# Kernel tuning notes

Hardware: AMD Instinct MI355X
Metric: run time of the kernel (lower is better)

## Reference

```python
import jax, jax.numpy as jnp
import numpy as np

D_MODEL = 1024
N_HEADS = 16
D_K = D_MODEL // N_HEADS


def setup_inputs() -> dict:
    key = jax.random.key(0)
    ks = jax.random.split(key, 9)
    s = 1.0 / np.sqrt(D_MODEL)
    x = jax.random.normal(ks[0], (2, 2048, D_MODEL), dtype=jnp.float32)
    Wq = jax.random.uniform(ks[1], (D_MODEL, D_MODEL), jnp.float32, -s, s)
    bq = jax.random.uniform(ks[2], (D_MODEL,), jnp.float32, -s, s)
    Wk = jax.random.uniform(ks[3], (D_MODEL, D_MODEL), jnp.float32, -s, s)
    bk = jax.random.uniform(ks[4], (D_MODEL,), jnp.float32, -s, s)
    Wv = jax.random.uniform(ks[5], (D_MODEL, D_MODEL), jnp.float32, -s, s)
    bv = jax.random.uniform(ks[6], (D_MODEL,), jnp.float32, -s, s)
    Wo = jax.random.uniform(ks[7], (D_MODEL, D_MODEL), jnp.float32, -s, s)
    bo = jax.random.uniform(ks[8], (D_MODEL,), jnp.float32, -s, s)
    return {"x": x, "Wq": Wq, "bq": bq, "Wk": Wk, "bk": bk,
            "Wv": Wv, "bv": bv, "Wo": Wo, "bo": bo}


def reference(x, Wq, bq, Wk, bk, Wv, bv, Wo, bo):
    B, S, _ = x.shape
    # torch Linear: y = x @ W.T + b
    def proj(W, b):
        h = x @ W.T + b                       # [B,S,D]
        return h.reshape(B, S, N_HEADS, D_K).transpose(0, 2, 1, 3)  # [B,H,S,dk]
    Q, K, V = proj(Wq, bq), proj(Wk, bk), proj(Wv, bv)
    scale = 1.0 / np.sqrt(D_K).astype(np.float32)
    scores = jnp.einsum('bhqd,bhkd->bhqk', Q, K) * scale  # [B,H,S,S]
    causal = jnp.tril(jnp.ones((S, S), dtype=bool))
    scores = jnp.where(causal, scores, -jnp.inf)
    attn = jax.nn.softmax(scores, axis=-1)
    ctx = jnp.einsum('bhqk,bhkd->bhqd', attn, V)          # [B,H,S,dk]
    ctx = ctx.transpose(0, 2, 1, 3).reshape(B, S, D_MODEL)
    return ctx @ Wo.T + bo
```

## Files before the change

### kernel.cpp

```cpp
#include <hip/hip_runtime.h>
#include <stdint.h>

#define D_MODEL 1024
#define NHEADS  16
#define DKH     64
#define BATCH   2
#define SEQ     2048
#define NTOK    (BATCH*SEQ)

typedef unsigned short u16;
typedef __attribute__((ext_vector_type(8))) short short8;
typedef __attribute__((ext_vector_type(4))) float f32x4;
typedef __attribute__((address_space(1))) unsigned int as1_u32;
typedef __attribute__((address_space(3))) unsigned int as3_u32;

__device__ __forceinline__ u16 f2bf(float f) {
  unsigned int i = __float_as_uint(f);
  i += 0x7FFF + ((i >> 16) & 1);
  return (u16)(i >> 16);
}
__device__ __forceinline__ f32x4 mfma_bf16(short8 a, short8 b, f32x4 c) {
  return __builtin_amdgcn_mfma_f32_16x16x32_bf16(a, b, c, 0, 0, 0);
}
__device__ __forceinline__ void gload_lds16(const u16* g, u16* l) {
  __builtin_amdgcn_global_load_lds((as1_u32*)g, (as3_u32*)l, 16, 0, 0);
}
__device__ __forceinline__ short8 ld_frag(const u16* p) {
  short8 v; __builtin_memcpy(&v, __builtin_assume_aligned(p, 16), 16); return v;
}
__device__ __forceinline__ void ld16(uint32_t* dst4, const void* src) {
  __builtin_memcpy(dst4, __builtin_assume_aligned(src, 16), 16);
}
__device__ __forceinline__ void st16(u16* dst, const uint32_t* src4) {
  __builtin_memcpy(__builtin_assume_aligned(dst, 16), src4, 16);
}
__device__ __forceinline__ uint32_t pk_bf16_trunc(float hi, float lo) {
  return __builtin_amdgcn_perm(__float_as_uint(hi), __float_as_uint(lo), 0x07060302u);
}

#define QSCALE 0.18033688011112042f
#define M0LOG2 4.32808512266689f

__global__ __launch_bounds__(256)
void convert_kernel(const float* __restrict__ x,  const float* __restrict__ wq,
                    const float* __restrict__ wk, const float* __restrict__ wv,
                    const float* __restrict__ wo,
                    u16* __restrict__ xb,  u16* __restrict__ wqb,
                    u16* __restrict__ wkb, u16* __restrict__ wvb,
                    u16* __restrict__ wob)
{
  const int q = blockIdx.x * 256 + threadIdx.x;
  const float* src; u16* dst; int local;
  if (q < 1048576) { src = x; dst = xb; local = q; }
  else {
    const int t = q - 1048576, r = t >> 18;
    local = t & 262143;
    src = (r == 0) ? wq : (r == 1) ? wk : (r == 2) ? wv : wo;
    dst = (r == 0) ? wqb : (r == 1) ? wkb : (r == 2) ? wvb : wob;
  }
  float f[4];
  __builtin_memcpy(f, src + (size_t)local * 4, 16);
  uint32_t o[2];
  o[0] = ((uint32_t)f2bf(f[1]) << 16) | f2bf(f[0]);
  o[1] = ((uint32_t)f2bf(f[3]) << 16) | f2bf(f[2]);
  __builtin_memcpy(dst + (size_t)local * 4, o, 8);
}

__device__ __forceinline__ void gemm_core_bf16(
    const u16* __restrict__ A, const u16* __restrict__ Bt,
    int m0, int n0, u16* As, u16* Bs, f32x4 (&acc)[4][4])
{
  const int tid  = threadIdx.x;
  const int wave = tid >> 6, lane = tid & 63;
  const int quad = lane >> 4, l15 = lane & 15;
  const int wm = wave & 1, wn = wave >> 1;
  const int srow = lane >> 2;
  const int scol = (lane & 3) << 3;

#pragma unroll
  for (int i = 0; i < 4; i++)
#pragma unroll
    for (int j = 0; j < 4; j++) acc[i][j] = (f32x4){0.f, 0.f, 0.f, 0.f};

  for (int k0 = 0; k0 < D_MODEL; k0 += 32) {
    __syncthreads();
#pragma unroll
    for (int is = 0; is < 2; is++) {
      const int rbase = (is * 4 + wave) * 16;
      gload_lds16(A  + (size_t)(m0 + rbase + srow) * D_MODEL + k0 + scol, As + rbase * 32);
      gload_lds16(Bt + (size_t)(n0 + rbase + srow) * D_MODEL + k0 + scol, Bs + rbase * 32);
    }
    __syncthreads();

    short8 aF[4], bF[4];
#pragma unroll
    for (int i = 0; i < 4; i++)
      aF[i] = ld_frag(As + (wm * 64 + i * 16 + l15) * 32 + quad * 8);
#pragma unroll
    for (int j = 0; j < 4; j++)
      bF[j] = ld_frag(Bs + (wn * 64 + j * 16 + l15) * 32 + quad * 8);
#pragma unroll
    for (int i = 0; i < 4; i++)
#pragma unroll
      for (int j = 0; j < 4; j++)
        acc[i][j] = mfma_bf16(aF[i], bF[j], acc[i][j]);
  }
}

__global__ __launch_bounds__(256)
void qkv_proj_kernel(const u16* __restrict__ xb,
                     const u16* __restrict__ Wqb, const u16* __restrict__ Wkb,
                     const u16* __restrict__ Wvb,
                     const float* __restrict__ bq, const float* __restrict__ bk,
                     const float* __restrict__ bv,
                     u16* __restrict__ qplane, u16* __restrict__ ws)
{
  __shared__ __align__(16) u16 As[128 * 32];
  __shared__ __align__(16) u16 Bs[128 * 32];

  const int m0  = blockIdx.x * 128;
  const int by  = blockIdx.y;
  const int mat = by >> 3;
  const int n0  = (by & 7) * 128;
  const u16* W      = (mat == 0) ? Wqb : (mat == 1) ? Wkb : Wvb;
  const float* bias = (mat == 0) ? bq : (mat == 1) ? bk : bv;
  u16* out = (mat == 0) ? qplane : ws + (size_t)(mat - 1) * ((size_t)NTOK * D_MODEL);
  const float scale = (mat == 0) ? QSCALE : 1.0f;

  f32x4 acc[4][4];
  gemm_core_bf16(xb, W, m0, n0, As, Bs, acc);

  const int tid = threadIdx.x, wave = tid >> 6, lane = tid & 63;
  const int quad = lane >> 4, l15 = lane & 15;
  const int wm = wave & 1, wn = wave >> 1;
#pragma unroll
  for (int j = 0; j < 4; j++) {
    const int gcol = n0 + wn * 64 + j * 16 + l15;
    const float bias_v = bias[gcol];
    const int h = gcol >> 6, dj = gcol & 63;
#pragma unroll
    for (int i = 0; i < 4; i++) {
#pragma unroll
      for (int r = 0; r < 4; r++) {
        const int grow = m0 + wm * 64 + i * 16 + quad * 4 + r;
        const int b = grow >> 11, s = grow & (SEQ - 1);
        const float v = (acc[i][j][r] + bias_v) * scale;
        out[(((size_t)(b * NHEADS + h)) * SEQ + s) * DKH + dj] = f2bf(v);
      }
    }
  }
}

#define LP 72

__device__ __forceinline__ void storeVt(u16* Vt, const uint32_t* va,
                                        const uint32_t* vb, int r2, int cV) {
#pragma unroll
  for (int j = 0; j < 8; j++) {
    const uint32_t lo = (va[j >> 1] >> (16 * (j & 1))) & 0xFFFFu;
    const uint32_t hi = (vb[j >> 1] >> (16 * (j & 1))) & 0xFFFFu;
    const uint32_t w = (hi << 16) | lo;
    __builtin_memcpy(Vt + (size_t)(cV + j) * LP + r2, &w, 4);
  }
}

__global__ __launch_bounds__(512, 4)
void attn_kernel(const u16* __restrict__ Qp, const u16* __restrict__ Kp,
                 const u16* __restrict__ Vp, u16* __restrict__ ctx)
{
  __shared__ __align__(16) u16 Ks[2][64 * LP];
  __shared__ __align__(16) u16 Vts[2][64 * LP];
  __shared__ __align__(16) u16 PsB[2][64 * LP];
  __shared__ float Ls[2][64];

  const int xp = blockIdx.x;
  const int bh = blockIdx.y;
  const u16* Q = Qp + (size_t)bh * SEQ * DKH;
  const u16* K = Kp + (size_t)bh * SEQ * DKH;
  const u16* V = Vp + (size_t)bh * SEQ * DKH;

  const int tid = threadIdx.x;
  const int wave = tid >> 6, lane = tid & 63;
  const int quad = lane >> 4, l15 = lane & 15;
  const int g    = tid >> 8;
  const int qw   = wave & 3;
  const int ktid = tid & 255;
  const int rK = ktid & 63, cK = (ktid >> 6) * 16;
  const int r2 = (ktid & 31) * 2, cV = (ktid >> 5) * 8;
  const int qloc = qw * 16 + l15;
  const int b = bh >> 4, h = bh & 15;
  u16* Psg = PsB[g];
  float* Osum = (float*)(&PsB[0][0]);

#pragma unroll
  for (int p = 0; p < 2; p++) {
    const int qt = p ? xp : 31 - xp;
    const int q0 = qt * 64;
    const int maxR = (qt >> 1) + 1;

    const short8 qf0 = ld_frag(Q + (size_t)(q0 + qw * 16 + l15) * DKH + quad * 8);
    const short8 qf1 = ld_frag(Q + (size_t)(q0 + qw * 16 + l15) * DKH + 32 + quad * 8);

    uint32_t ka[4], kb[4], va[4], vb[4];
    const bool act0 = (g <= qt);
    if (act0) {
      const int k0 = g * 64;
      ld16(ka, K + (size_t)(k0 + rK) * DKH + cK);
      ld16(kb, K + (size_t)(k0 + rK) * DKH + cK + 8);
      ld16(va, V + (size_t)(k0 + r2) * DKH + cV);
      ld16(vb, V + (size_t)(k0 + r2 + 1) * DKH + cV);
    }
    __syncthreads();
    if (act0) {
      st16(Ks[g] + rK * LP + cK,     ka);
      st16(Ks[g] + rK * LP + cK + 8, kb);
      storeVt(Vts[g], va, vb, r2, cV);
    }
    float l_acc = 0.f;
    f32x4 oacc[4];
#pragma unroll
    for (int td = 0; td < 4; td++) oacc[td] = (f32x4){0.f, 0.f, 0.f, 0.f};
    __syncthreads();

    for (int r = 0; r < maxR; r++) {
      const int kt = 2 * r + g;
      const bool act = (kt <= qt);
      const bool pre = (kt + 2 <= qt);
      if (pre) {
        const int kn = (kt + 2) * 64;
        ld16(ka, K + (size_t)(kn + rK) * DKH + cK);
        ld16(kb, K + (size_t)(kn + rK) * DKH + cK + 8);
        ld16(va, V + (size_t)(kn + r2) * DKH + cV);
        ld16(vb, V + (size_t)(kn + r2 + 1) * DKH + cV);
      }
      if (act) {
        f32x4 sacc[4];
#pragma unroll
        for (int tk = 0; tk < 4; tk++)
          sacc[tk] = (f32x4){-M0LOG2, -M0LOG2, -M0LOG2, -M0LOG2};
#pragma unroll
        for (int tk = 0; tk < 4; tk++) {
          const short8 kf0 = ld_frag(Ks[g] + (tk * 16 + l15) * LP + 0  + quad * 8);
          sacc[tk] = mfma_bf16(kf0, qf0, sacc[tk]);
          const short8 kf1 = ld_frag(Ks[g] + (tk * 16 + l15) * LP + 32 + quad * 8);
          sacc[tk] = mfma_bf16(kf1, qf1, sacc[tk]);
        }
        const bool diag = (kt == qt);
#pragma unroll
        for (int tk = 0; tk < 4; tk++) {
          float pr[4];
#pragma unroll
          for (int rg = 0; rg < 4; rg++) {
            float pv = exp2f(sacc[tk][rg]);
            if (diag) {
              const int kloc = tk * 16 + quad * 4 + rg;
              if (kloc > qloc) pv = 0.f;
            }
            pr[rg] = pv; l_acc += pv;
          }
          uint32_t w[2];
          w[0] = pk_bf16_trunc(pr[1], pr[0]);
          w[1] = pk_bf16_trunc(pr[3], pr[2]);
          __builtin_memcpy(__builtin_assume_aligned(
              Psg + (size_t)(qw * 16 + l15) * LP + tk * 16 + quad * 4, 8), w, 8);
        }
#pragma unroll
        for (int kk = 0; kk < 2; kk++) {
          const short8 pf = ld_frag(Psg + (size_t)(qw * 16 + l15) * LP + kk * 32 + quad * 8);
#pragma unroll
          for (int td = 0; td < 4; td++) {
            const short8 vf = ld_frag(Vts[g] + (size_t)(td * 16 + l15) * LP + kk * 32 + quad * 8);
            oacc[td] = mfma_bf16(pf, vf, oacc[td]);
          }
        }
      }
      if (r + 1 < maxR) {
        __syncthreads();
        if (pre) {
          st16(Ks[g] + rK * LP + cK,     ka);
          st16(Ks[g] + rK * LP + cK + 8, kb);
          storeVt(Vts[g], va, vb, r2, cV);
        }
        __syncthreads();
      }
    }

    l_acc += __shfl_xor(l_acc, 16);
    l_acc += __shfl_xor(l_acc, 32);
    if (quad == 0) Ls[g][qw * 16 + l15] = l_acc;
    __syncthreads();
    if (g == 0) {
#pragma unroll
      for (int td = 0; td < 4; td++)
#pragma unroll
        for (int rg = 0; rg < 4; rg++)
          Osum[(qw * 16 + quad * 4 + rg) * 65 + td * 16 + l15] = oacc[td][rg];
    }
    __syncthreads();
    if (g == 1) {
#pragma unroll
      for (int rg = 0; rg < 4; rg++) {
        const int qrow = qw * 16 + quad * 4 + rg;
        const float inv = 1.0f / (Ls[0][qrow] + Ls[1][qrow]);
        const int sq = q0 + qrow;
#pragma unroll
        for (int td = 0; td < 4; td++) {
          const int dcol = td * 16 + l15;
          const float v = (oacc[td][rg] + Osum[qrow * 65 + dcol]) * inv;
          ctx[((size_t)(b * SEQ + sq)) * D_MODEL + h * DKH + dcol] = f2bf(v);
        }
      }
    }
  }
}

__global__ __launch_bounds__(256)
void oproj_kernel(const u16* __restrict__ ctx, const u16* __restrict__ Wob,
                  const float* __restrict__ bo, float* __restrict__ out)
{
  __shared__ __align__(16) u16 As[128 * 32];
  __shared__ __align__(16) u16 Bs[128 * 32];
  const int m0 = blockIdx.x * 128, n0 = blockIdx.y * 128;

  f32x4 acc[4][4];
  gemm_core_bf16(ctx, Wob, m0, n0, As, Bs, acc);

  const int tid = threadIdx.x, wave = tid >> 6, lane = tid & 63;
  const int quad = lane >> 4, l15 = lane & 15;
  const int wm = wave & 1, wn = wave >> 1;
#pragma unroll
  for (int j = 0; j < 4; j++) {
    const int gcol = n0 + wn * 64 + j * 16 + l15;
    const float bias_v = bo[gcol];
#pragma unroll
    for (int i = 0; i < 4; i++) {
#pragma unroll
      for (int r = 0; r < 4; r++) {
        const int grow = m0 + wm * 64 + i * 16 + quad * 4 + r;
        out[(size_t)grow * D_MODEL + gcol] = acc[i][j][r] + bias_v;
      }
    }
  }
}

extern "C" void kernel_launch(void* const* d_in, const int* in_sizes, int n_in,
                              void* d_out, int out_size, void* d_ws, size_t ws_size,
                              hipStream_t stream) {
  const float* x  = (const float*)d_in[0];
  const float* Wq = (const float*)d_in[1];
  const float* bq = (const float*)d_in[2];
  const float* Wk = (const float*)d_in[3];
  const float* bk = (const float*)d_in[4];
  const float* Wv = (const float*)d_in[5];
  const float* bv = (const float*)d_in[6];
  const float* Wo = (const float*)d_in[7];
  const float* bo = (const float*)d_in[8];
  u16*   ws   = (u16*)d_ws;
  u16*   o16  = (u16*)d_out;
  float* out  = (float*)d_out;

  const size_t plane = (size_t)NTOK * D_MODEL;
  u16* Kp  = ws;
  u16* Vp  = ws + plane;
  u16* xb  = ws + 2 * plane;
  u16* ctx = ws + 2 * plane;
  u16* Wob = ws + 3 * plane;
  u16* Qp  = o16;
  u16* Wqb = o16 + 4 * 1048576;
  u16* Wkb = o16 + 5 * 1048576;
  u16* Wvb = o16 + 6 * 1048576;

  convert_kernel<<<dim3(8192), dim3(256), 0, stream>>>(x, Wq, Wk, Wv, Wo,
                                                       xb, Wqb, Wkb, Wvb, Wob);
  qkv_proj_kernel<<<dim3(32, 24), dim3(256), 0, stream>>>(xb, Wqb, Wkb, Wvb,
                                                          bq, bk, bv, Qp, ws);
  attn_kernel<<<dim3(16, 32), dim3(512), 0, stream>>>(Qp, Kp, Vp, ctx);
  oproj_kernel<<<dim3(32, 8), dim3(256), 0, stream>>>(ctx, Wob, bo, out);
}
```

Before: 209.6 us.

## Restructure attention to 32x32 MFMA with 4-way key split and swizzled LDS

```diff
diff --git a/kernel.cpp b/kernel.cpp
--- a/kernel.cpp
+++ b/kernel.cpp
@@ -11,6 +11,8 @@
 typedef unsigned short u16;
 typedef __attribute__((ext_vector_type(8))) short short8;
 typedef __attribute__((ext_vector_type(4))) float f32x4;
+typedef __attribute__((ext_vector_type(16))) float f32x16;
+typedef __attribute__((ext_vector_type(2))) unsigned int u32x2;
 typedef __attribute__((address_space(1))) unsigned int as1_u32;
 typedef __attribute__((address_space(3))) unsigned int as3_u32;
 
@@ -21,6 +23,9 @@
 }
 __device__ __forceinline__ f32x4 mfma_bf16(short8 a, short8 b, f32x4 c) {
   return __builtin_amdgcn_mfma_f32_16x16x32_bf16(a, b, c, 0, 0, 0);
+}
+__device__ __forceinline__ f32x16 mfma32(short8 a, short8 b, f32x16 c) {
+  return __builtin_amdgcn_mfma_f32_32x32x16_bf16(a, b, c, 0, 0, 0);
 }
 __device__ __forceinline__ void gload_lds16(const u16* g, u16* l) {
   __builtin_amdgcn_global_load_lds((as1_u32*)g, (as3_u32*)l, 16, 0, 0);
@@ -151,16 +156,64 @@
   }
 }
 
-#define LP 72
 
 __device__ __forceinline__ void storeVt(u16* Vt, const uint32_t* va,
                                         const uint32_t* vb, int r2, int cV) {
 #pragma unroll
   for (int j = 0; j < 8; j++) {
+    const int d = cV + j;
     const uint32_t lo = (va[j >> 1] >> (16 * (j & 1))) & 0xFFFFu;
     const uint32_t hi = (vb[j >> 1] >> (16 * (j & 1))) & 0xFFFFu;
     const uint32_t w = (hi << 16) | lo;
-    __builtin_memcpy(Vt + (size_t)(cV + j) * LP + r2, &w, 4);
+    __builtin_memcpy(Vt + d * 64 + (r2 ^ ((d & 7) << 3)), &w, 4);
+  }
+}
+
+__device__ __forceinline__ void soft_pack(const f32x16& s, const int khBase,
+                                          const bool diag, const int qloc,
+                                          const int h4, float& l_acc,
+                                          short8& fA, short8& fB) {
+  float pv[16];
+#pragma unroll
+  for (int rr = 0; rr < 16; rr++) {
+    float v = exp2f(s[rr]);
+    if (diag) {
+      const int kloc = khBase + (rr & 3) + 8 * (rr >> 2) + h4;
+      if (kloc > qloc) v = 0.f;
+    }
+    pv[rr] = v; l_acc += v;
+  }
+  uint32_t w[2][4];
+#pragma unroll
+  for (int ks = 0; ks < 2; ks++) {
+    const uint32_t x0 = pk_bf16_trunc(pv[8 * ks + 1], pv[8 * ks + 0]);
+    const uint32_t x1 = pk_bf16_trunc(pv[8 * ks + 3], pv[8 * ks + 2]);
+    const uint32_t y0 = pk_bf16_trunc(pv[8 * ks + 5], pv[8 * ks + 4]);
+    const uint32_t y1 = pk_bf16_trunc(pv[8 * ks + 7], pv[8 * ks + 6]);
+    const u32x2 r0 = __builtin_amdgcn_permlane32_swap(x0, y0, false, false);
+    const u32x2 r1 = __builtin_amdgcn_permlane32_swap(x1, y1, false, false);
+    w[ks][0] = r0[0]; w[ks][1] = r1[0]; w[ks][2] = r0[1]; w[ks][3] = r1[1];
+  }
+  __builtin_memcpy(&fA, &w[0][0], 16);
+  __builtin_memcpy(&fB, &w[1][0], 16);
+}
+
+__device__ __forceinline__ void osum_write(float* OS, const f32x16& o0,
+                                           const f32x16& o1, int qb, int l31) {
+#pragma unroll
+  for (int rr = 0; rr < 16; rr++) {
+    const int q = qb + (rr & 3) + 8 * (rr >> 2);
+    OS[q * 64 + l31]      = o0[rr];
+    OS[q * 64 + 32 + l31] = o1[rr];
+  }
+}
+__device__ __forceinline__ void osum_add(const float* OS, f32x16& o0,
+                                         f32x16& o1, int qb, int l31) {
+#pragma unroll
+  for (int rr = 0; rr < 16; rr++) {
+    const int q = qb + (rr & 3) + 8 * (rr >> 2);
+    o0[rr] += OS[q * 64 + l31];
+    o1[rr] += OS[q * 64 + 32 + l31];
   }
 }
 
@@ -168,10 +221,8 @@
 void attn_kernel(const u16* __restrict__ Qp, const u16* __restrict__ Kp,
                  const u16* __restrict__ Vp, u16* __restrict__ ctx)
 {
-  __shared__ __align__(16) u16 Ks[2][64 * LP];
-  __shared__ __align__(16) u16 Vts[2][64 * LP];
-  __shared__ __align__(16) u16 PsB[2][64 * LP];
-  __shared__ float Ls[2][64];
+  __shared__ __align__(16) u16 Ks[4][64 * 64];
+  __shared__ __align__(16) u16 Vts[4][64 * 64];
 
   const int xp = blockIdx.x;
   const int bh = blockIdx.y;
@@ -179,136 +230,138 @@
   const u16* K = Kp + (size_t)bh * SEQ * DKH;
   const u16* V = Vp + (size_t)bh * SEQ * DKH;
 
-  const int tid = threadIdx.x;
-  const int wave = tid >> 6, lane = tid & 63;
-  const int quad = lane >> 4, l15 = lane & 15;
-  const int g    = tid >> 8;
-  const int qw   = wave & 3;
-  const int ktid = tid & 255;
-  const int rK = ktid & 63, cK = (ktid >> 6) * 16;
-  const int r2 = (ktid & 31) * 2, cV = (ktid >> 5) * 8;
-  const int qloc = qw * 16 + l15;
-  const int b = bh >> 4, h = bh & 15;
-  u16* Psg = PsB[g];
-  float* Osum = (float*)(&PsB[0][0]);
+  const int tid  = threadIdx.x;
+  const int lane = tid & 63;
+  const int l31  = lane & 31, h = lane >> 5;
+  const int g    = tid >> 7;
+  const int wq   = (tid >> 6) & 1;
+  const int ktid = tid & 127;
+  const int rK = ktid & 63, c0 = (ktid >> 6) * 8;
+  const int r2 = (ktid & 31) * 2, cV = ((ktid >> 5) & 3) * 8;
+  const int b = bh >> 4, hd = bh & 15;
+  const int qloc = wq * 32 + l31;
+  const int qb   = wq * 32 + h * 4;
+  const int xr   = (l31 & 7) << 3;
+  const int krx  = (rK & 7) << 3;
+  const int h8   = h * 8;
+
+  u16* ksg = &Ks[g][0];
+  u16* vtg = &Vts[g][0];
+  float* Osum0 = (float*)&Ks[0][0];
+  float* Osum1 = (float*)&Ks[2][0];
+  float* Ls    = (float*)&Vts[0][0];
 
 #pragma unroll
   for (int p = 0; p < 2; p++) {
     const int qt = p ? xp : 31 - xp;
     const int q0 = qt * 64;
-    const int maxR = (qt >> 1) + 1;
-
-    const short8 qf0 = ld_frag(Q + (size_t)(q0 + qw * 16 + l15) * DKH + quad * 8);
-    const short8 qf1 = ld_frag(Q + (size_t)(q0 + qw * 16 + l15) * DKH + 32 + quad * 8);
-
-    uint32_t ka[4], kb[4], va[4], vb[4];
+    const int maxR = (qt >> 2) + 1;
+
+    uint32_t ka[4][4], va[4], vb[4], vc[4], vd[4];
     const bool act0 = (g <= qt);
     if (act0) {
-      const int k0 = g * 64;
-      ld16(ka, K + (size_t)(k0 + rK) * DKH + cK);
-      ld16(kb, K + (size_t)(k0 + rK) * DKH + cK + 8);
-      ld16(va, V + (size_t)(k0 + r2) * DKH + cV);
-      ld16(vb, V + (size_t)(k0 + r2 + 1) * DKH + cV);
+      const int kn = g * 64;
+#pragma unroll
+      for (int i = 0; i < 4; i++)
+        ld16(ka[i], K + (size_t)(kn + rK) * DKH + c0 + i * 16);
+      ld16(va, V + (size_t)(kn + r2) * DKH + cV);
+      ld16(vb, V + (size_t)(kn + r2 + 1) * DKH + cV);
+      ld16(vc, V + (size_t)(kn + r2) * DKH + cV + 32);
+      ld16(vd, V + (size_t)(kn + r2 + 1) * DKH + cV + 32);
     }
     __syncthreads();
     if (act0) {
-      st16(Ks[g] + rK * LP + cK,     ka);
-      st16(Ks[g] + rK * LP + cK + 8, kb);
-      storeVt(Vts[g], va, vb, r2, cV);
+#pragma unroll
+      for (int i = 0; i < 4; i++)
+        st16(ksg + rK * 64 + ((c0 + i * 16) ^ krx), ka[i]);
+      storeVt(vtg, va, vb, r2, cV);
+      storeVt(vtg, vc, vd, r2, cV + 32);
     }
     float l_acc = 0.f;
-    f32x4 oacc[4];
-#pragma unroll
-    for (int td = 0; td < 4; td++) oacc[td] = (f32x4){0.f, 0.f, 0.f, 0.f};
+    f32x16 oacc0, oacc1;
+#pragma unroll
+    for (int rr = 0; rr < 16; rr++) { oacc0[rr] = 0.f; oacc1[rr] = 0.f; }
     __syncthreads();
 
     for (int r = 0; r < maxR; r++) {
-      const int kt = 2 * r + g;
+      const int kt = 4 * r + g;
       const bool act = (kt <= qt);
-      const bool pre = (kt + 2 <= qt);
+      const bool pre = (kt + 4 <= qt);
       if (pre) {
-        const int kn = (kt + 2) * 64;
-        ld16(ka, K + (size_t)(kn + rK) * DKH + cK);
-        ld16(kb, K + (size_t)(kn + rK) * DKH + cK + 8);
+        const int kn = (kt + 4) * 64;
+#pragma unroll
+        for (int i = 0; i < 4; i++)
+          ld16(ka[i], K + (size_t)(kn + rK) * DKH + c0 + i * 16);
         ld16(va, V + (size_t)(kn + r2) * DKH + cV);
         ld16(vb, V + (size_t)(kn + r2 + 1) * DKH + cV);
+        ld16(vc, V + (size_t)(kn + r2) * DKH + cV + 32);
+        ld16(vd, V + (size_t)(kn + r2 + 1) * DKH + cV + 32);
       }
       if (act) {
-        f32x4 sacc[4];
-#pragma unroll
-        for (int tk = 0; tk < 4; tk++)
-          sacc[tk] = (f32x4){-M0LOG2, -M0LOG2, -M0LOG2, -M0LOG2};
-#pragma unroll
-        for (int tk = 0; tk < 4; tk++) {
-          const short8 kf0 = ld_frag(Ks[g] + (tk * 16 + l15) * LP + 0  + quad * 8);
-          sacc[tk] = mfma_bf16(kf0, qf0, sacc[tk]);
-          const short8 kf1 = ld_frag(Ks[g] + (tk * 16 + l15) * LP + 32 + quad * 8);
-          sacc[tk] = mfma_bf16(kf1, qf1, sacc[tk]);
-        }
+        short8 qf0 = ld_frag(Q + (size_t)(q0 + qloc) * DKH + 0  + h8);
+        short8 qf1 = ld_frag(Q + (size_t)(q0 + qloc) * DKH + 16 + h8);
+        short8 qf2 = ld_frag(Q + (size_t)(q0 + qloc) * DKH + 32 + h8);
+        short8 qf3 = ld_frag(Q + (size_t)(q0 + qloc) * DKH + 48 + h8);
+        f32x16 s0, s1;
+#pragma unroll
+        for (int rr = 0; rr < 16; rr++) { s0[rr] = -M0LOG2; s1[rr] = -M0LOG2; }
+        s0 = mfma32(ld_frag(ksg + l31 * 64        + ((0  + h8) ^ xr)), qf0, s0);
+        s1 = mfma32(ld_frag(ksg + (32 + l31) * 64 + ((0  + h8) ^ xr)), qf0, s1);
+        s0 = mfma32(ld_frag(ksg + l31 * 64        + ((16 + h8) ^ xr)), qf1, s0);
+        s1 = mfma32(ld_frag(ksg + (32 + l31) * 64 + ((16 + h8) ^ xr)), qf1, s1);
+        s0 = mfma32(ld_frag(ksg + l31 * 64        + ((32 + h8) ^ xr)), qf2, s0);
+        s1 = mfma32(ld_frag(ksg + (32 + l31) * 64 + ((32 + h8) ^ xr)), qf2, s1);
+        s0 = mfma32(ld_frag(ksg + l31 * 64        + ((48 + h8) ^ xr)), qf3, s0);
+        s1 = mfma32(ld_frag(ksg + (32 + l31) * 64 + ((48 + h8) ^ xr)), qf3, s1);
         const bool diag = (kt == qt);
-#pragma unroll
-        for (int tk = 0; tk < 4; tk++) {
-          float pr[4];
-#pragma unroll
-          for (int rg = 0; rg < 4; rg++) {
-            float pv = exp2f(sacc[tk][rg]);
-            if (diag) {
-              const int kloc = tk * 16 + quad * 4 + rg;
-              if (kloc > qloc) pv = 0.f;
-            }
-            pr[rg] = pv; l_acc += pv;
-          }
-          uint32_t w[2];
-          w[0] = pk_bf16_trunc(pr[1], pr[0]);
-          w[1] = pk_bf16_trunc(pr[3], pr[2]);
-          __builtin_memcpy(__builtin_assume_aligned(
-              Psg + (size_t)(qw * 16 + l15) * LP + tk * 16 + quad * 4, 8), w, 8);
-        }
-#pragma unroll
-        for (int kk = 0; kk < 2; kk++) {
-          const short8 pf = ld_frag(Psg + (size_t)(qw * 16 + l15) * LP + kk * 32 + quad * 8);
-#pragma unroll
-          for (int td = 0; td < 4; td++) {
-            const short8 vf = ld_frag(Vts[g] + (size_t)(td * 16 + l15) * LP + kk * 32 + quad * 8);
-            oacc[td] = mfma_bf16(pf, vf, oacc[td]);
-          }
-        }
+        short8 pa0, pa1, pa2, pa3;
+        soft_pack(s0, 0,  diag, qloc, h * 4, l_acc, pa0, pa1);
+        soft_pack(s1, 32, diag, qloc, h * 4, l_acc, pa2, pa3);
+        oacc0 = mfma32(pa0, ld_frag(vtg + l31 * 64        + ((0  + h8) ^ xr)), oacc0);
+        oacc1 = mfma32(pa0, ld_frag(vtg + (32 + l31) * 64 + ((0  + h8) ^ xr)), oacc1);
+        oacc0 = mfma32(pa1, ld_frag(vtg + l31 * 64        + ((16 + h8) ^ xr)), oacc0);
+        oacc1 = mfma32(pa1, ld_frag(vtg + (32 + l31) * 64 + ((16 + h8) ^ xr)), oacc1);
+        oacc0 = mfma32(pa2, ld_frag(vtg + l31 * 64        + ((32 + h8) ^ xr)), oacc0);
+        oacc1 = mfma32(pa2, ld_frag(vtg + (32 + l31) * 64 + ((32 + h8) ^ xr)), oacc1);
+        oacc0 = mfma32(pa3, ld_frag(vtg + l31 * 64        + ((48 + h8) ^ xr)), oacc0);
+        oacc1 = mfma32(pa3, ld_frag(vtg + (32 + l31) * 64 + ((48 + h8) ^ xr)), oacc1);
       }
       if (r + 1 < maxR) {
         __syncthreads();
         if (pre) {
-          st16(Ks[g] + rK * LP + cK,     ka);
-          st16(Ks[g] + rK * LP + cK + 8, kb);
-          storeVt(Vts[g], va, vb, r2, cV);
+#pragma unroll
+          for (int i = 0; i < 4; i++)
+            st16(ksg + rK * 64 + ((c0 + i * 16) ^ krx), ka[i]);
+          storeVt(vtg, va, vb, r2, cV);
+          storeVt(vtg, vc, vd, r2, cV + 32);
         }
         __syncthreads();
       }
     }
 
-    l_acc += __shfl_xor(l_acc, 16);
     l_acc += __shfl_xor(l_acc, 32);
-    if (quad == 0) Ls[g][qw * 16 + l15] = l_acc;
+    __syncthreads();
+    if (lane < 32) Ls[g * 64 + wq * 32 + l31] = l_acc;
+    if (g == 1) osum_write(Osum0, oacc0, oacc1, qb, l31);
+    if (g == 3) osum_write(Osum1, oacc0, oacc1, qb, l31);
+    __syncthreads();
+    if (g == 0) osum_add(Osum0, oacc0, oacc1, qb, l31);
+    if (g == 2) osum_add(Osum1, oacc0, oacc1, qb, l31);
+    if ((tid >> 6) == 2) {
+      const float s = Ls[lane] + Ls[64 + lane] + Ls[128 + lane] + Ls[192 + lane];
+      Ls[lane] = 1.f / s;
+    }
+    __syncthreads();
+    if (g == 2) osum_write(Osum0, oacc0, oacc1, qb, l31);
     __syncthreads();
     if (g == 0) {
 #pragma unroll
-      for (int td = 0; td < 4; td++)
-#pragma unroll
-        for (int rg = 0; rg < 4; rg++)
-          Osum[(qw * 16 + quad * 4 + rg) * 65 + td * 16 + l15] = oacc[td][rg];
-    }
-    __syncthreads();
-    if (g == 1) {
-#pragma unroll
-      for (int rg = 0; rg < 4; rg++) {
-        const int qrow = qw * 16 + quad * 4 + rg;
-        const float inv = 1.0f / (Ls[0][qrow] + Ls[1][qrow]);
-        const int sq = q0 + qrow;
-#pragma unroll
-        for (int td = 0; td < 4; td++) {
-          const int dcol = td * 16 + l15;
-          const float v = (oacc[td][rg] + Osum[qrow * 65 + dcol]) * inv;
-          ctx[((size_t)(b * SEQ + sq)) * D_MODEL + h * DKH + dcol] = f2bf(v);
-        }
+      for (int rr = 0; rr < 16; rr++) {
+        const int q = qb + (rr & 3) + 8 * (rr >> 2);
+        const float linv = Ls[q];
+        u16* dst = ctx + ((size_t)(b * SEQ + q0 + q)) * D_MODEL + hd * DKH;
+        dst[l31]      = f2bf((oacc0[rr] + Osum0[q * 64 + l31]) * linv);
+        dst[32 + l31] = f2bf((oacc1[rr] + Osum0[q * 64 + 32 + l31]) * linv);
       }
     }
   }
```

Result: slower. 268.9 us (+28.3%).
